# Optimization experiments

Hardware: AMD Instinct MI355X
Metric: run time of the kernel (lower is better)

The kernel has to match this reference:

```python
import jax, jax.numpy as jnp
import numpy as np

# Grid config: xbound [0,90,0.6], ybound [-15,15,0.15], zbound [-10,10,20]
DX = np.array([0.6, 0.15, 20.0], dtype=np.float32)                 # voxel sizes
BX = np.array([0.0 + 0.3, -15.0 + 0.075, -10.0 + 10.0], dtype=np.float32)  # voxel-center origins
NX = (150, 200, 1)                                                 # voxels per axis


def setup_inputs() -> dict:
    key = jax.random.key(0)
    k1, k2, k3, k4 = jax.random.split(key, 4)
    B, N, D, H, W, C = 4, 6, 59, 16, 44, 64
    shp = (B, N, D, H, W)
    # ego-frame frustum point coordinates; ranges slightly exceed grid bounds
    gx = jax.random.uniform(k1, shp, jnp.float32, minval=-2.0, maxval=95.0)
    gy = jax.random.uniform(k2, shp, jnp.float32, minval=-17.0, maxval=17.0)
    gz = jax.random.uniform(k3, shp, jnp.float32, minval=-3.0, maxval=3.0)
    geom_feats = jnp.stack([gx, gy, gz], axis=-1)                  # [B,N,D,H,W,3]
    x = jax.random.normal(k4, shp + (C,), jnp.float32)             # [B,N,D,H,W,C]
    return {"geom_feats": geom_feats, "x": x}


def reference(geom_feats, x):
    """LSS voxel_pooling. The torch sort + cumsum + diff (QuickCumsum) computes the
    per-voxel sum of features; here expressed as a masked segment_sum (same math)."""
    B, N, D, H, W, C = x.shape
    Nprime = B * N * D * H * W
    nx0, nx1, nx2 = NX

    xf = x.reshape(Nprime, C)
    dx = jnp.asarray(DX)
    bx = jnp.asarray(BX)
    # torch .long() truncates toward zero; astype(int32) matches that
    g = ((geom_feats - (bx - dx / 2.0)) / dx).astype(jnp.int32).reshape(Nprime, 3)

    batch_ix = jnp.repeat(jnp.arange(B, dtype=jnp.int32), Nprime // B)  # [Nprime]

    kept = ((g[:, 0] >= 0) & (g[:, 0] < nx0)
            & (g[:, 1] >= 0) & (g[:, 1] < nx1)
            & (g[:, 2] >= 0) & (g[:, 2] < nx2))

    ranks = (g[:, 0] * (nx1 * nx2 * B)
             + g[:, 1] * (nx2 * B)
             + g[:, 2] * B
             + batch_ix)
    total = nx0 * nx1 * nx2 * B
    seg = jnp.where(kept, ranks, total)  # dropped points -> dummy segment

    pooled = jax.ops.segment_sum(jnp.where(kept[:, None], xf, 0.0), seg,
                                 num_segments=total + 1)[:total]   # [nx0*nx1*nx2*B, C]

    final = pooled.reshape(nx0, nx1, nx2, B, C).transpose(3, 4, 2, 0, 1)  # [B,C,Z,X,Y]
    # torch.cat(final.unbind(dim=2), 1) -> [B, C*Z, X, Y]
    out = jnp.concatenate([final[:, :, z] for z in range(nx2)], axis=1)
    return out
```

## Files before the change

### kernel.cpp

```cpp
#include <hip/hip_runtime.h>


#define NPRIME 996864
#define NCH 64
#define NX0 150
#define NX1 200
#define CELLS_PER_B (NX0 * NX1)
#define NCELLS (4 * CELLS_PER_B)
#define BATCH_STRIDE (NPRIME / 4)
#define CAP 44
#define CNT_BYTES ((size_t)NCELLS * 4)
#define SLOT_BYTES ((size_t)NCELLS * CAP * 4)
#define ACC_BYTES ((size_t)NCELLS * NCH * 4)
#define CELL_BYTES ((size_t)NPRIME * 4)

__device__ __forceinline__ int bin_recip(float v, float off, float rcp) {
    float num = v - off;
    float q   = num * rcp;
    return (int)q;
}

__device__ __forceinline__ int compute_cell(float gx, float gy, float gz, int p) {
    int i0 = bin_recip(gx,   0.0f, 1.0f / 0.6f);
    int i1 = bin_recip(gy, -15.0f, 1.0f / 0.15f);
    int i2 = bin_recip(gz, -10.0f, 1.0f / 20.0f);
    bool kept = (i0 >= 0) & (i0 < NX0) & (i1 >= 0) & (i1 < NX1) & (i2 >= 0) & (i2 < 1);
    int b = p / BATCH_STRIDE;
    return kept ? (b * CELLS_PER_B + i0 * NX1 + i1) : -1;
}

__global__ __launch_bounds__(256) void lss_bin_push(
    const float* __restrict__ geom,
    unsigned* __restrict__ cnt,
    int* __restrict__ slots)
{
    int p = blockIdx.x * 256 + threadIdx.x;
    if (p >= NPRIME) return;
    float gx = geom[3 * p + 0];
    float gy = geom[3 * p + 1];
    float gz = geom[3 * p + 2];
    int c = compute_cell(gx, gy, gz, p);
    if (c < 0) return;
    unsigned pos = atomicAdd(&cnt[c], 1u);
    if (pos < CAP) slots[c * CAP + pos] = p;
}

__global__ __launch_bounds__(1024) void lss_accum(
    const float* __restrict__ x,
    const unsigned* __restrict__ cnt,
    const int* __restrict__ slots,
    float* __restrict__ out)
{
    __shared__ float tile[64][65];
    int b    = blockIdx.y;
    int xy0  = blockIdx.x * 64;
    int t    = threadIdx.x;
    int wave = t >> 6;
    int lane = t & 63;

    #pragma unroll
    for (int j = 0; j < 4; ++j) {
        int xyl = wave * 4 + j;
        int xy  = xy0 + xyl;
        float acc0 = 0.0f, acc1 = 0.0f;
        if (xy < CELLS_PER_B) {
            int cell = b * CELLS_PER_B + xy;
            int n = (int)cnt[cell];
            if (n > CAP) n = CAP;
            const int* sl = slots + (size_t)cell * CAP;
            int i = 0;
            for (; i + 1 < n; i += 2) {
                int p0 = sl[i];
                int p1 = sl[i + 1];
                acc0 += x[(size_t)p0 * NCH + lane];
                acc1 += x[(size_t)p1 * NCH + lane];
            }
            if (i < n) acc0 += x[(size_t)sl[i] * NCH + lane];
        }
        tile[xyl][lane] = acc0 + acc1;
    }
    __syncthreads();

    int c   = t >> 4;
    int xyl = (t & 15) * 4;
    int xy  = xy0 + xyl;
    if (xy + 3 < CELLS_PER_B) {
        float4 w;
        w.x = tile[xyl + 0][c];
        w.y = tile[xyl + 1][c];
        w.z = tile[xyl + 2][c];
        w.w = tile[xyl + 3][c];
        *reinterpret_cast<float4*>(out + ((size_t)(b * NCH + c)) * CELLS_PER_B + xy) = w;
    }
}

__global__ __launch_bounds__(256) void lss_bin(
    const float* __restrict__ geom, int* __restrict__ cell)
{
    int p = blockIdx.x * 256 + threadIdx.x;
    if (p >= NPRIME) return;
    cell[p] = compute_cell(geom[3 * p], geom[3 * p + 1], geom[3 * p + 2], p);
}

__global__ __launch_bounds__(256) void lss_scatter_direct(
    const float* __restrict__ x, const int* __restrict__ cell,
    float* __restrict__ out)
{
    int t = blockIdx.x * 256 + threadIdx.x;
    int p = t >> 4;
    if (p >= NPRIME) return;
    int c = cell[p];
    if (c < 0) return;
    int c4 = (t & 15) << 2;
    const float4 xv = *reinterpret_cast<const float4*>(x + (size_t)p * NCH + c4);
    int b  = c / CELLS_PER_B;
    int xy = c - b * CELLS_PER_B;
    float* o = out + ((size_t)(b * NCH + c4)) * CELLS_PER_B + xy;
    atomicAdd(o,                   xv.x);
    atomicAdd(o +     CELLS_PER_B, xv.y);
    atomicAdd(o + 2 * CELLS_PER_B, xv.z);
    atomicAdd(o + 3 * CELLS_PER_B, xv.w);
}

__global__ __launch_bounds__(256) void lss_fused(
    const float* __restrict__ geom, const float* __restrict__ x,
    float* __restrict__ out)
{
    int t = blockIdx.x * 256 + threadIdx.x;
    int p = t >> 4;
    if (p >= NPRIME) return;
    int c = compute_cell(geom[3 * p], geom[3 * p + 1], geom[3 * p + 2], p);
    if (c < 0) return;
    int b  = c / CELLS_PER_B;
    int xy = c - b * CELLS_PER_B;
    int c4 = (t & 15) << 2;
    const float4 xv = *reinterpret_cast<const float4*>(x + (size_t)p * NCH + c4);
    float* o = out + ((size_t)(b * NCH + c4)) * CELLS_PER_B + xy;
    atomicAdd(o,                   xv.x);
    atomicAdd(o +     CELLS_PER_B, xv.y);
    atomicAdd(o + 2 * CELLS_PER_B, xv.z);
    atomicAdd(o + 3 * CELLS_PER_B, xv.w);
}

extern "C" void kernel_launch(void* const* d_in, const int* in_sizes, int n_in,
                              void* d_out, int out_size, void* d_ws, size_t ws_size,
                              hipStream_t stream) {
    const float* geom = (const float*)d_in[0];
    const float* x    = (const float*)d_in[1];
    float* out = (float*)d_out;

    const int bin_blocks = (NPRIME + 255) / 256;

    if (ws_size >= CNT_BYTES + SLOT_BYTES) {
        unsigned* cnt = (unsigned*)d_ws;
        int* slots    = (int*)((char*)d_ws + CNT_BYTES);
        hipMemsetAsync(cnt, 0, CNT_BYTES, stream);
        lss_bin_push<<<bin_blocks, 256, 0, stream>>>(geom, cnt, slots);
        dim3 agrid((CELLS_PER_B + 63) / 64, 4);
        lss_accum<<<agrid, 1024, 0, stream>>>(x, cnt, slots, out);
    } else if (ws_size >= CELL_BYTES) {
        int* cell = (int*)d_ws;
        hipMemsetAsync(d_out, 0, (size_t)out_size * sizeof(float), stream);
        lss_bin<<<bin_blocks, 256, 0, stream>>>(geom, cell);
        lss_scatter_direct<<<(NPRIME * 16 + 255) / 256, 256, 0, stream>>>(x, cell, out);
    } else {
        hipMemsetAsync(d_out, 0, (size_t)out_size * sizeof(float), stream);
        lss_fused<<<(NPRIME * 16 + 255) / 256, 256, 0, stream>>>(geom, x, out);
    }
}
```

Before: 145.8 us.

## Interleave two cells per wave with 4-way unrolled gathers; replace memset with kernel

The accumulation kernel now gives each wave two cells instead of four processed one after another. It walks both slot lists together, unrolled by four with clamped indices and predicated adds, so that up to eight independent x gathers are in flight per iteration. The block tile shrinks to 32 cells, which doubles the grid, and only half the threads take part in the transposed store. The count memset becomes a small zero kernel to avoid hipMemsetAsync overhead. Padded lanes still issue loads of slot 0, so some redundant gather traffic is added.

```diff
diff --git a/kernel.cpp b/kernel.cpp
--- a/kernel.cpp
+++ b/kernel.cpp
@@ -11,7 +11,6 @@
 #define CAP 44
 #define CNT_BYTES ((size_t)NCELLS * 4)
 #define SLOT_BYTES ((size_t)NCELLS * CAP * 4)
-#define ACC_BYTES ((size_t)NCELLS * NCH * 4)
 #define CELL_BYTES ((size_t)NPRIME * 4)
 
 __device__ __forceinline__ int bin_recip(float v, float off, float rcp) {
@@ -29,6 +28,11 @@
     return kept ? (b * CELLS_PER_B + i0 * NX1 + i1) : -1;
 }
 
+__global__ __launch_bounds__(256) void lss_zero(unsigned* __restrict__ cnt) {
+    int i = blockIdx.x * 256 + threadIdx.x;
+    if (i < NCELLS) cnt[i] = 0u;
+}
+
 __global__ __launch_bounds__(256) void lss_bin_push(
     const float* __restrict__ geom,
     unsigned* __restrict__ cnt,
@@ -51,46 +55,77 @@
     const int* __restrict__ slots,
     float* __restrict__ out)
 {
-    __shared__ float tile[64][65];
+    __shared__ float tile[32][65];
     int b    = blockIdx.y;
-    int xy0  = blockIdx.x * 64;
+    int xy0  = blockIdx.x * 32;
     int t    = threadIdx.x;
     int wave = t >> 6;
     int lane = t & 63;
 
-    #pragma unroll
-    for (int j = 0; j < 4; ++j) {
-        int xyl = wave * 4 + j;
+    int xyA = xy0 + wave * 2;
+    int xyB = xyA + 1;
+    int cellA = b * CELLS_PER_B + xyA;
+    int cellB = b * CELLS_PER_B + xyB;
+    int nA = (xyA < CELLS_PER_B) ? (int)cnt[cellA] : 0;
+    int nB = (xyB < CELLS_PER_B) ? (int)cnt[cellB] : 0;
+    nA = nA > CAP ? CAP : nA;
+    nB = nB > CAP ? CAP : nB;
+    const int* slA = slots + (size_t)cellA * CAP;
+    const int* slB = slots + (size_t)cellB * CAP;
+
+    float aA0 = 0, aA1 = 0, aA2 = 0, aA3 = 0;
+    float aB0 = 0, aB1 = 0, aB2 = 0, aB3 = 0;
+    int nmax = nA > nB ? nA : nB;
+    for (int i = 0; i < nmax; i += 4) {
+        int jA0 = (i + 0 < nA) ? i + 0 : 0;
+        int jA1 = (i + 1 < nA) ? i + 1 : 0;
+        int jA2 = (i + 2 < nA) ? i + 2 : 0;
+        int jA3 = (i + 3 < nA) ? i + 3 : 0;
+        int jB0 = (i + 0 < nB) ? i + 0 : 0;
+        int jB1 = (i + 1 < nB) ? i + 1 : 0;
+        int jB2 = (i + 2 < nB) ? i + 2 : 0;
+        int jB3 = (i + 3 < nB) ? i + 3 : 0;
+        unsigned pA0 = min((unsigned)slA[jA0], NPRIME - 1u);
+        unsigned pA1 = min((unsigned)slA[jA1], NPRIME - 1u);
+        unsigned pA2 = min((unsigned)slA[jA2], NPRIME - 1u);
+        unsigned pA3 = min((unsigned)slA[jA3], NPRIME - 1u);
+        unsigned pB0 = min((unsigned)slB[jB0], NPRIME - 1u);
+        unsigned pB1 = min((unsigned)slB[jB1], NPRIME - 1u);
+        unsigned pB2 = min((unsigned)slB[jB2], NPRIME - 1u);
+        unsigned pB3 = min((unsigned)slB[jB3], NPRIME - 1u);
+        float vA0 = x[(size_t)pA0 * NCH + lane];
+        float vA1 = x[(size_t)pA1 * NCH + lane];
+        float vA2 = x[(size_t)pA2 * NCH + lane];
+        float vA3 = x[(size_t)pA3 * NCH + lane];
+        float vB0 = x[(size_t)pB0 * NCH + lane];
+        float vB1 = x[(size_t)pB1 * NCH + lane];
+        float vB2 = x[(size_t)pB2 * NCH + lane];
+        float vB3 = x[(size_t)pB3 * NCH + lane];
+        aA0 += (i + 0 < nA) ? vA0 : 0.0f;
+        aA1 += (i + 1 < nA) ? vA1 : 0.0f;
+        aA2 += (i + 2 < nA) ? vA2 : 0.0f;
+        aA3 += (i + 3 < nA) ? vA3 : 0.0f;
+        aB0 += (i + 0 < nB) ? vB0 : 0.0f;
+        aB1 += (i + 1 < nB) ? vB1 : 0.0f;
+        aB2 += (i + 2 < nB) ? vB2 : 0.0f;
+        aB3 += (i + 3 < nB) ? vB3 : 0.0f;
+    }
+    tile[wave * 2 + 0][lane] = (aA0 + aA1) + (aA2 + aA3);
+    tile[wave * 2 + 1][lane] = (aB0 + aB1) + (aB2 + aB3);
+    __syncthreads();
+
+    if (t < 512) {
+        int c   = t >> 3;
+        int xyl = (t & 7) * 4;
         int xy  = xy0 + xyl;
-        float acc0 = 0.0f, acc1 = 0.0f;
-        if (xy < CELLS_PER_B) {
-            int cell = b * CELLS_PER_B + xy;
-            int n = (int)cnt[cell];
-            if (n > CAP) n = CAP;
-            const int* sl = slots + (size_t)cell * CAP;
-            int i = 0;
-            for (; i + 1 < n; i += 2) {
-                int p0 = sl[i];
-                int p1 = sl[i + 1];
-                acc0 += x[(size_t)p0 * NCH + lane];
-                acc1 += x[(size_t)p1 * NCH + lane];
-            }
-            if (i < n) acc0 += x[(size_t)sl[i] * NCH + lane];
+        if (xy + 3 < CELLS_PER_B) {
+            float4 w;
+            w.x = tile[xyl + 0][c];
+            w.y = tile[xyl + 1][c];
+            w.z = tile[xyl + 2][c];
+            w.w = tile[xyl + 3][c];
+            *reinterpret_cast<float4*>(out + ((size_t)(b * NCH + c)) * CELLS_PER_B + xy) = w;
         }
-        tile[xyl][lane] = acc0 + acc1;
-    }
-    __syncthreads();
-
-    int c   = t >> 4;
-    int xyl = (t & 15) * 4;
-    int xy  = xy0 + xyl;
-    if (xy + 3 < CELLS_PER_B) {
-        float4 w;
-        w.x = tile[xyl + 0][c];
-        w.y = tile[xyl + 1][c];
-        w.z = tile[xyl + 2][c];
-        w.w = tile[xyl + 3][c];
-        *reinterpret_cast<float4*>(out + ((size_t)(b * NCH + c)) * CELLS_PER_B + xy) = w;
     }
 }
 
@@ -154,9 +189,9 @@
     if (ws_size >= CNT_BYTES + SLOT_BYTES) {
         unsigned* cnt = (unsigned*)d_ws;
         int* slots    = (int*)((char*)d_ws + CNT_BYTES);
-        hipMemsetAsync(cnt, 0, CNT_BYTES, stream);
+        lss_zero<<<(NCELLS + 255) / 256, 256, 0, stream>>>(cnt);
         lss_bin_push<<<bin_blocks, 256, 0, stream>>>(geom, cnt, slots);
-        dim3 agrid((CELLS_PER_B + 63) / 64, 4);
+        dim3 agrid((CELLS_PER_B + 31) / 32, 4);
         lss_accum<<<agrid, 1024, 0, stream>>>(x, cnt, slots, out);
     } else if (ws_size >= CELL_BYTES) {
         int* cell = (int*)d_ws;
```

After: 117.6 us (median of 2 runs). 19.4% less time.
